# Performance work log

Hardware: AMD Instinct MI355X
Metric: run time of the kernel (lower is better)

The kernel has to match this reference:

```python
import jax, jax.numpy as jnp
import numpy as np

B, T, S, D = 32, 1024, 1024, 512
VOCAB = 1000
INSERT_TOK = jnp.array([1, 2], dtype=jnp.int64)


def setup_inputs() -> dict:
    key = jax.random.key(0)
    k1, k2, k3, k4, k5 = jax.random.split(key, 5)
    input_var = jax.random.randint(k1, (B, T), 0, VOCAB, dtype=jnp.int64)
    output = jax.random.normal(k2, (B, T, D), jnp.float32)
    context = jax.random.normal(k3, (B, S, D), jnp.float32)
    # nn.Linear(2*dim, dim): weight [D, 2D], bias [D]
    W = jax.random.normal(k4, (D, 2 * D), jnp.float32) / np.sqrt(2 * D)
    b = jax.random.normal(k5, (D,), jnp.float32) * 0.01
    return {"input_var": input_var, "output": output, "context": context,
            "di": 0, "W": W, "b": b}


def _hard_align(input_var, src_len):
    """Replicates the python double-loop: sequential 'inserted' counter per batch.
    Returns (j, valid): j[b,i] = column of the 1.0 in attn row i (torch negative
    indices wrapped), valid[b,i] = whether row i gets any 1.0 at all."""
    bsz, tgt_len = input_var.shape
    flags = jnp.isin(input_var, INSERT_TOK)  # [B,T] is token an insert token

    def step(inserted, xi):
        i, flag = xi  # i: scalar position, flag: [B]
        cond = (src_len >= i - inserted)                    # gate, per batch
        ins2 = inserted + jnp.where(cond & flag, 1, 0)      # increment before write
        j = i - ins2 - 1
        j = jnp.where(j < 0, j + src_len, j)                # torch negative-index wrap
        return ins2, (j, cond)

    idxs = jnp.arange(1, tgt_len, dtype=jnp.int32)
    init = jnp.zeros((bsz,), jnp.int32)  # init_inserted()
    _, (j_rows, valid) = jax.lax.scan(step, init, (idxs, flags[:, 1:].T))
    j_rows = j_rows.T      # [B,T-1]
    valid = valid.T        # [B,T-1]
    # row 0: attn[b,0,0] = 1.0 always
    j_full = jnp.concatenate([jnp.zeros((bsz, 1), j_rows.dtype), j_rows], axis=1)
    valid_full = jnp.concatenate([jnp.ones((bsz, 1), bool), valid], axis=1)
    return j_full, valid_full


def reference(input_var, output, context, di, W, b):
    bsz, tgt_len, hid = output.shape
    src_len = context.shape[1]
    j, valid = _hard_align(input_var, src_len)              # [B,T], [B,T]
    vf = valid[:, :, None].astype(output.dtype)
    # hard one-hot attention matrix (as the module materializes it)
    attn = jax.nn.one_hot(j, src_len, dtype=output.dtype) * vf  # [B,T,S]
    # mix = bmm(attn, context) == masked gather of context rows
    mix = jnp.take_along_axis(context, j[:, :, None].astype(jnp.int32), axis=1) * vf
    combined = jnp.concatenate([mix, output], axis=-1)      # [B,T,2D]
    out = jnp.tanh(combined @ W.T + b)                      # [B,T,D]
    return out, attn
```

## Files before the change

### kernel.cpp

```cpp
#include <hip/hip_runtime.h>
#include <hip/hip_bf16.h>

#define B_ 32
#define T_ 1024
#define S_ 1024
#define D_ 512
#define M_ (B_*T_)
#define N_ D_
#define K_ (2*D_)

typedef __attribute__((ext_vector_type(8))) short bf16x8;
typedef __attribute__((ext_vector_type(4))) float f32x4;

__device__ inline unsigned short f2bf(float x) {
    union { float f; unsigned u; } v; v.f = x;
    unsigned r = v.u + 0x7FFFu + ((v.u >> 16) & 1u);
    return (unsigned short)(r >> 16);
}

__device__ inline unsigned cvt2bf(float lo, float hi) {
#if __has_builtin(__builtin_amdgcn_cvt_pk_bf16_f32)
    typedef __attribute__((ext_vector_type(2))) __bf16 bf2;
    union { bf2 v; unsigned u; } r;
    r.v = __builtin_amdgcn_cvt_pk_bf16_f32(lo, hi);
    return r.u;
#else
    return (unsigned)f2bf(lo) | ((unsigned)f2bf(hi) << 16);
#endif
}

__device__ inline float fast_tanh(float x) {
#if __has_builtin(__builtin_amdgcn_exp2f) && __has_builtin(__builtin_amdgcn_rcpf)
    const float e = __builtin_amdgcn_exp2f(x * 2.885390082f);
    const float r = __builtin_amdgcn_rcpf(e + 1.0f);
    return 1.0f - 2.0f * r;
#else
    return tanhf(x);
#endif
}

__global__ void align_kernel(const int* __restrict__ iv, int* __restrict__ jbuf) {
    const int b = blockIdx.x;
    const int lane = threadIdx.x;
    const int* row = iv + b * T_;
    int f[16];
    int local = 0;
    const int t0 = lane * 16;
    #pragma unroll
    for (int q = 0; q < 16; ++q) {
        const int t = t0 + q;
        const int tok = row[t];
        const int fl = (t > 0 && (tok == 1 || tok == 2)) ? 1 : 0;
        f[q] = fl;
        local += fl;
    }
    int incl = local;
    #pragma unroll
    for (int off = 1; off < 64; off <<= 1) {
        const int up = __shfl_up(incl, off, 64);
        if (lane >= off) incl += up;
    }
    int run = incl - local;
    #pragma unroll
    for (int q = 0; q < 16; ++q) {
        const int t = t0 + q;
        run += f[q];
        int j;
        if (t == 0) {
            j = 0;
        } else {
            j = t - run - 1;
            if (j < 0) j += S_;
        }
        jbuf[b * T_ + t] = j;
    }
}

__global__ void pack_w(const float* __restrict__ W, unsigned short* __restrict__ Wbf) {
    const int idx = blockIdx.x * blockDim.x + threadIdx.x;
    const f32x4 a = ((const f32x4*)W)[idx * 2];
    const f32x4 c = ((const f32x4*)W)[idx * 2 + 1];
    union { bf16x8 v; unsigned u[4]; } pk;
    pk.u[0] = cvt2bf(a[0], a[1]); pk.u[1] = cvt2bf(a[2], a[3]);
    pk.u[2] = cvt2bf(c[0], c[1]); pk.u[3] = cvt2bf(c[2], c[3]);
    *(bf16x8*)(Wbf + (size_t)idx * 8) = pk.v;
}

#define BM 128
#define BN 128
#define BK 64
#define NIT (K_ / BK)
#define KMAX (K_ - BK)
#define NGEMM ((M_ / BM) * (N_ / BN))
#define NATTN 512

__global__ __launch_bounds__(256, 2)
void gemm_attn(const unsigned short* __restrict__ Wbf,
               const float* __restrict__ bias,
               float* __restrict__ out,
               float* __restrict__ attn,
               const float* __restrict__ ctx,
               const float* __restrict__ outp,
               const int* __restrict__ jbuf) {
    const int bx = blockIdx.x;
    const int tid = threadIdx.x;

    if (bx < NATTN) {
        const int m0 = bx * 64;
        #pragma unroll 4
        for (int r = 0; r < 64; ++r) {
            const int row = m0 + r;
            const int j = jbuf[row];
            f32x4 v = {0.f, 0.f, 0.f, 0.f};
            if ((j >> 2) == tid) v[j & 3] = 1.0f;
            __builtin_nontemporal_store(v, ((f32x4*)(attn + (size_t)row * S_)) + tid);
        }
        return;
    }

    __shared__ unsigned short As[2][BM * BK];
    __shared__ unsigned short Bs[2][BN * BK];

    const int gbx  = bx - NATTN;
    const int lane = tid & 63;
    const int wave = tid >> 6;
    const int wm = wave >> 1, wn = wave & 1;
    const int l16 = lane & 15, quad = lane >> 4;

    const int bm = gbx & 255;
    const int bn = gbx >> 8;
    const int mBase = bm * BM;
    const int nBase = bn * BN;

    const int kc   = tid & 7;
    const int rsub = tid >> 3;
    const int sw   = kc ^ (rsub & 7);
    const float* actx[4];
    const float* aout[4];
    #pragma unroll
    for (int it = 0; it < 4; ++it) {
        const int r = it * 32 + rsub;
        const int m = mBase + r;
        const int jm = jbuf[m];
        actx[it] = ctx + ((size_t)((m >> 10) * S_ + jm)) * D_ + kc * 8;
        aout[it] = outp + (size_t)m * D_ - D_ + kc * 8;
    }

    f32x4 acc[4][4] = {};
    f32x4 fa0[4][2], fa1[4][2];

#define LOAD_A(FA, KO) do {                                                    \
    const int _koa = (KO);                                                     \
    _Pragma("unroll")                                                          \
    for (int _it = 0; _it < 4; ++_it) {                                        \
        const float* _src = (_koa < D_) ? (actx[_it] + _koa) : (aout[_it] + _koa); \
        FA[_it][0] = ((const f32x4*)_src)[0];                                  \
        FA[_it][1] = ((const f32x4*)_src)[1];                                  \
    }                                                                          \
} while (0)

#define DMA_B(PP, KO) do {                                                     \
    const int _kob = (KO);                                                     \
    _Pragma("unroll")                                                          \
    for (int _it = 0; _it < 4; ++_it) {                                        \
        const int _chunk = _it * 256 + tid;                                    \
        const int _row = _chunk >> 3;                                          \
        const int _kcb = _chunk & 7;                                           \
        const int _gk8 = (_kcb ^ (_row & 7)) * 8;                              \
        const unsigned short* _gB = Wbf + (size_t)(nBase + _row) * K_ + _kob + _gk8; \
        __builtin_amdgcn_global_load_lds(                                      \
            (const __attribute__((address_space(1))) void*)_gB,                \
            (__attribute__((address_space(3))) void*)(&Bs[PP][_chunk * 8]), 16, 0, 0); \
    }                                                                          \
} while (0)

#define STAGE_A(PP, FA) do {                                                   \
    _Pragma("unroll")                                                          \
    for (int _it = 0; _it < 4; ++_it) {                                        \
        union { bf16x8 v; unsigned u[4]; } _pk;                                \
        _pk.u[0] = cvt2bf(FA[_it][0][0], FA[_it][0][1]);                       \
        _pk.u[1] = cvt2bf(FA[_it][0][2], FA[_it][0][3]);                       \
        _pk.u[2] = cvt2bf(FA[_it][1][0], FA[_it][1][1]);                       \
        _pk.u[3] = cvt2bf(FA[_it][1][2], FA[_it][1][3]);                       \
        *(bf16x8*)&As[PP][(_it * 256 + rsub * 8 + sw) * 8] = _pk.v;            \
    }                                                                          \
} while (0)

#define MFMA_PH(PP) do {                                                       \
    _Pragma("unroll")                                                          \
    for (int _ks = 0; _ks < 2; ++_ks) {                                        \
        bf16x8 _af[4], _bfr[4];                                                \
        _Pragma("unroll")                                                      \
        for (int _mt = 0; _mt < 4; ++_mt) {                                    \
            const int _r = wm * 64 + _mt * 16 + l16;                           \
            const int _q = _ks * 4 + quad;                                     \
            _af[_mt] = *(const bf16x8*)&As[PP][(_r * 8 + (_q ^ (_r & 7))) * 8]; \
        }                                                                      \
        _Pragma("unroll")                                                      \
        for (int _nt = 0; _nt < 4; ++_nt) {                                    \
            const int _r = wn * 64 + _nt * 16 + l16;                           \
            const int _q = _ks * 4 + quad;                                     \
            _bfr[_nt] = *(const bf16x8*)&Bs[PP][(_r * 8 + (_q ^ (_r & 7))) * 8]; \
        }                                                                      \
        _Pragma("unroll")                                                      \
        for (int _mt = 0; _mt < 4; ++_mt)                                      \
            _Pragma("unroll")                                                  \
            for (int _nt = 0; _nt < 4; ++_nt)                                  \
                acc[_mt][_nt] = __builtin_amdgcn_mfma_f32_16x16x32_bf16(       \
                    _af[_mt], _bfr[_nt], acc[_mt][_nt], 0, 0, 0);              \
    }                                                                          \
} while (0)

    LOAD_A(fa0, 0);
    DMA_B(0, 0);
    __builtin_amdgcn_sched_barrier(0);
    LOAD_A(fa1, BK);
    __builtin_amdgcn_sched_barrier(0);
    STAGE_A(0, fa0);
    asm volatile("s_waitcnt vmcnt(8) lgkmcnt(0)" ::: "memory");
    __builtin_amdgcn_sched_barrier(0);
    __builtin_amdgcn_s_barrier();

    #pragma unroll 1
    for (int i = 0; i < NIT; i += 2) {
        const int ko = i * BK;
        DMA_B(1, ko + BK);
        __builtin_amdgcn_sched_barrier(0);
        {
            const int _ka = (ko + 2 * BK > KMAX) ? KMAX : ko + 2 * BK;
            LOAD_A(fa0, _ka);
        }
        __builtin_amdgcn_sched_barrier(0);
        STAGE_A(1, fa1);
        MFMA_PH(0);
        asm volatile("s_waitcnt vmcnt(8) lgkmcnt(0)" ::: "memory");
        __builtin_amdgcn_sched_barrier(0);
        __builtin_amdgcn_s_barrier();

        {
            const int _kb = (ko + 2 * BK > KMAX) ? KMAX : ko + 2 * BK;
            DMA_B(0, _kb);
        }
        __builtin_amdgcn_sched_barrier(0);
        {
            const int _kcl = (ko + 3 * BK > KMAX) ? KMAX : ko + 3 * BK;
            LOAD_A(fa1, _kcl);
        }
        __builtin_amdgcn_sched_barrier(0);
        STAGE_A(0, fa0);
        MFMA_PH(1);
        asm volatile("s_waitcnt vmcnt(8) lgkmcnt(0)" ::: "memory");
        __builtin_amdgcn_sched_barrier(0);
        __builtin_amdgcn_s_barrier();
    }

#undef LOAD_A
#undef DMA_B
#undef STAGE_A
#undef MFMA_PH

    #pragma unroll
    for (int nt = 0; nt < 4; ++nt) {
        const int n = nBase + wn * 64 + nt * 16 + l16;
        const float bv = bias[n];
        #pragma unroll
        for (int mt = 0; mt < 4; ++mt) {
            #pragma unroll
            for (int r = 0; r < 4; ++r) {
                const int m = mBase + wm * 64 + mt * 16 + quad * 4 + r;
                const float val = fast_tanh(acc[mt][nt][r] + bv);
                __builtin_nontemporal_store(val, &out[(size_t)m * N_ + n]);
            }
        }
    }
}

extern "C" void kernel_launch(void* const* d_in, const int* in_sizes, int n_in,
                              void* d_out, int out_size, void* d_ws, size_t ws_size,
                              hipStream_t stream) {
    const int*   iv   = (const int*)d_in[0];
    const float* outp = (const float*)d_in[1];
    const float* ctx  = (const float*)d_in[2];
    const float* W    = (const float*)d_in[4];
    const float* bias = (const float*)d_in[5];

    float* out  = (float*)d_out;
    float* attn = out + (size_t)M_ * N_;

    int* jbuf = (int*)d_ws;
    unsigned short* Wbf = (unsigned short*)((char*)d_ws + (size_t)M_ * 4);

    align_kernel<<<B_, 64, 0, stream>>>(iv, jbuf);
    pack_w<<<(N_ * K_ / 8) / 256, 256, 0, stream>>>(W, Wbf);
    gemm_attn<<<NGEMM + NATTN, 256, 0, stream>>>(Wbf, bias, out, attn, ctx, outp, jbuf);
}
```

Baseline: 352.0 us.

## Single-buffer LDS to raise occupancy and fold attn writes into GEMM blocks

Replaces the double-buffered LDS tiles with a single buffer and raises the launch-bounds occupancy target from 2 to 4 blocks per CU. The loop is rescheduled to compute, barrier, then refill, with the register-staged A prefetch still in flight. The separate attention one-hot writer blocks are removed, and each GEMM block now writes 32 attn rows before its epilogue. This trades LDS-level overlap and extra barriers for more resident waves, and it spreads the large attn store stream across GEMM blocks.

```diff
diff --git a/kernel.cpp b/kernel.cpp
--- a/kernel.cpp
+++ b/kernel.cpp
@@ -92,9 +92,8 @@
 #define NIT (K_ / BK)
 #define KMAX (K_ - BK)
 #define NGEMM ((M_ / BM) * (N_ / BN))
-#define NATTN 512
-
-__global__ __launch_bounds__(256, 2)
+
+__global__ __launch_bounds__(256, 4)
 void gemm_attn(const unsigned short* __restrict__ Wbf,
                const float* __restrict__ bias,
                float* __restrict__ out,
@@ -102,26 +101,11 @@
                const float* __restrict__ ctx,
                const float* __restrict__ outp,
                const int* __restrict__ jbuf) {
-    const int bx = blockIdx.x;
+    __shared__ unsigned short As[BM * BK];
+    __shared__ unsigned short Bs[BN * BK];
+
+    const int gbx = blockIdx.x;
     const int tid = threadIdx.x;
-
-    if (bx < NATTN) {
-        const int m0 = bx * 64;
-        #pragma unroll 4
-        for (int r = 0; r < 64; ++r) {
-            const int row = m0 + r;
-            const int j = jbuf[row];
-            f32x4 v = {0.f, 0.f, 0.f, 0.f};
-            if ((j >> 2) == tid) v[j & 3] = 1.0f;
-            __builtin_nontemporal_store(v, ((f32x4*)(attn + (size_t)row * S_)) + tid);
-        }
-        return;
-    }
-
-    __shared__ unsigned short As[2][BM * BK];
-    __shared__ unsigned short Bs[2][BN * BK];
-
-    const int gbx  = bx - NATTN;
     const int lane = tid & 63;
     const int wave = tid >> 6;
     const int wm = wave >> 1, wn = wave & 1;
@@ -159,7 +143,7 @@
     }                                                                          \
 } while (0)
 
-#define DMA_B(PP, KO) do {                                                     \
+#define DMA_B(KO) do {                                                         \
     const int _kob = (KO);                                                     \
     _Pragma("unroll")                                                          \
     for (int _it = 0; _it < 4; ++_it) {                                        \
@@ -170,11 +154,11 @@
         const unsigned short* _gB = Wbf + (size_t)(nBase + _row) * K_ + _kob + _gk8; \
         __builtin_amdgcn_global_load_lds(                                      \
             (const __attribute__((address_space(1))) void*)_gB,                \
-            (__attribute__((address_space(3))) void*)(&Bs[PP][_chunk * 8]), 16, 0, 0); \
-    }                                                                          \
-} while (0)
-
-#define STAGE_A(PP, FA) do {                                                   \
+            (__attribute__((address_space(3))) void*)(&Bs[_chunk * 8]), 16, 0, 0); \
+    }                                                                          \
+} while (0)
+
+#define STAGE_A(FA) do {                                                       \
     _Pragma("unroll")                                                          \
     for (int _it = 0; _it < 4; ++_it) {                                        \
         union { bf16x8 v; unsigned u[4]; } _pk;                                \
@@ -182,11 +166,11 @@
         _pk.u[1] = cvt2bf(FA[_it][0][2], FA[_it][0][3]);                       \
         _pk.u[2] = cvt2bf(FA[_it][1][0], FA[_it][1][1]);                       \
         _pk.u[3] = cvt2bf(FA[_it][1][2], FA[_it][1][3]);                       \
-        *(bf16x8*)&As[PP][(_it * 256 + rsub * 8 + sw) * 8] = _pk.v;            \
-    }                                                                          \
-} while (0)
-
-#define MFMA_PH(PP) do {                                                       \
+        *(bf16x8*)&As[(_it * 256 + rsub * 8 + sw) * 8] = _pk.v;                \
+    }                                                                          \
+} while (0)
+
+#define MFMA_PH() do {                                                         \
     _Pragma("unroll")                                                          \
     for (int _ks = 0; _ks < 2; ++_ks) {                                        \
         bf16x8 _af[4], _bfr[4];                                                \
@@ -194,13 +178,13 @@
         for (int _mt = 0; _mt < 4; ++_mt) {                                    \
             const int _r = wm * 64 + _mt * 16 + l16;                           \
             const int _q = _ks * 4 + quad;                                     \
-            _af[_mt] = *(const bf16x8*)&As[PP][(_r * 8 + (_q ^ (_r & 7))) * 8]; \
+            _af[_mt] = *(const bf16x8*)&As[(_r * 8 + (_q ^ (_r & 7))) * 8];    \
         }                                                                      \
         _Pragma("unroll")                                                      \
         for (int _nt = 0; _nt < 4; ++_nt) {                                    \
             const int _r = wn * 64 + _nt * 16 + l16;                           \
             const int _q = _ks * 4 + quad;                                     \
-            _bfr[_nt] = *(const bf16x8*)&Bs[PP][(_r * 8 + (_q ^ (_r & 7))) * 8]; \
+            _bfr[_nt] = *(const bf16x8*)&Bs[(_r * 8 + (_q ^ (_r & 7))) * 8];   \
         }                                                                      \
         _Pragma("unroll")                                                      \
         for (int _mt = 0; _mt < 4; ++_mt)                                      \
@@ -212,11 +196,11 @@
 } while (0)
 
     LOAD_A(fa0, 0);
-    DMA_B(0, 0);
+    DMA_B(0);
     __builtin_amdgcn_sched_barrier(0);
     LOAD_A(fa1, BK);
     __builtin_amdgcn_sched_barrier(0);
-    STAGE_A(0, fa0);
+    STAGE_A(fa0);
     asm volatile("s_waitcnt vmcnt(8) lgkmcnt(0)" ::: "memory");
     __builtin_amdgcn_sched_barrier(0);
     __builtin_amdgcn_s_barrier();
@@ -224,40 +208,59 @@
     #pragma unroll 1
     for (int i = 0; i < NIT; i += 2) {
         const int ko = i * BK;
-        DMA_B(1, ko + BK);
+        MFMA_PH();
+        __builtin_amdgcn_s_barrier();
+        DMA_B(ko + BK);
         __builtin_amdgcn_sched_barrier(0);
         {
             const int _ka = (ko + 2 * BK > KMAX) ? KMAX : ko + 2 * BK;
             LOAD_A(fa0, _ka);
         }
         __builtin_amdgcn_sched_barrier(0);
-        STAGE_A(1, fa1);
-        MFMA_PH(0);
+        STAGE_A(fa1);
         asm volatile("s_waitcnt vmcnt(8) lgkmcnt(0)" ::: "memory");
         __builtin_amdgcn_sched_barrier(0);
         __builtin_amdgcn_s_barrier();
 
-        {
-            const int _kb = (ko + 2 * BK > KMAX) ? KMAX : ko + 2 * BK;
-            DMA_B(0, _kb);
-        }
-        __builtin_amdgcn_sched_barrier(0);
-        {
-            const int _kcl = (ko + 3 * BK > KMAX) ? KMAX : ko + 3 * BK;
-            LOAD_A(fa1, _kcl);
-        }
-        __builtin_amdgcn_sched_barrier(0);
-        STAGE_A(0, fa0);
-        MFMA_PH(1);
-        asm volatile("s_waitcnt vmcnt(8) lgkmcnt(0)" ::: "memory");
-        __builtin_amdgcn_sched_barrier(0);
-        __builtin_amdgcn_s_barrier();
+        MFMA_PH();
+        if (i != NIT - 2) {
+            __builtin_amdgcn_s_barrier();
+            DMA_B(ko + 2 * BK);
+            __builtin_amdgcn_sched_barrier(0);
+            LOAD_A(fa1, ko + 3 * BK);
+            __builtin_amdgcn_sched_barrier(0);
+            STAGE_A(fa0);
+            asm volatile("s_waitcnt vmcnt(8) lgkmcnt(0)" ::: "memory");
+            __builtin_amdgcn_sched_barrier(0);
+            __builtin_amdgcn_s_barrier();
+        }
     }
 
 #undef LOAD_A
 #undef DMA_B
 #undef STAGE_A
 #undef MFMA_PH
+
+    {
+        const int arow = gbx * 32 + (tid >> 3);
+        const int jv = jbuf[arow];
+        const int c4 = jv >> 2;
+        const bool hit = ((c4 & 7) == (tid & 7));
+        const int starget = c4 >> 3;
+        const int elem = jv & 3;
+        f32x4* abase = (f32x4*)(attn + (size_t)arow * S_);
+        #pragma unroll
+        for (int s = 0; s < 32; ++s) {
+            f32x4 v = {0.f, 0.f, 0.f, 0.f};
+            if (hit && s == starget) {
+                v[0] = (elem == 0) ? 1.f : 0.f;
+                v[1] = (elem == 1) ? 1.f : 0.f;
+                v[2] = (elem == 2) ? 1.f : 0.f;
+                v[3] = (elem == 3) ? 1.f : 0.f;
+            }
+            __builtin_nontemporal_store(v, abase + s * 8 + (tid & 7));
+        }
+    }
 
     #pragma unroll
     for (int nt = 0; nt < 4; ++nt) {
@@ -292,5 +295,5 @@
 
     align_kernel<<<B_, 64, 0, stream>>>(iv, jbuf);
     pack_w<<<(N_ * K_ / 8) / 256, 256, 0, stream>>>(W, Wbf);
-    gemm_attn<<<NGEMM + NATTN, 256, 0, stream>>>(Wbf, bias, out, attn, ctx, outp, jbuf);
-}
+    gemm_attn<<<NGEMM, 256, 0, stream>>>(Wbf, bias, out, attn, ctx, outp, jbuf);
+}
```

Result: slower. 422.0 us (+19.9%).

## Enlarge GEMM tiles to 256x256, fold attn one-hot writes into epilogue, XCD-aware block mapping

Applied to the files above, without the earlier changes.

Doubles the GEMM tile to 256x256 with 512 threads (8 waves, each computing 64x128), which halves how often A and B are reloaded across blocks. The separate attention-writing blocks are removed; each GEMM block now writes its share of the one-hot attn rows just before its output epilogue. Block indices are remapped so consecutive blocks spread across the 8 XCDs. The cost is heavier register pressure (the accumulator doubles) and much more LDS, which may lower occupancy, and there are only 256 blocks in total.

```diff
diff --git a/kernel.cpp b/kernel.cpp
--- a/kernel.cpp
+++ b/kernel.cpp
@@ -86,15 +86,14 @@
     *(bf16x8*)(Wbf + (size_t)idx * 8) = pk.v;
 }
 
-#define BM 128
-#define BN 128
+#define BM 256
+#define BN 256
 #define BK 64
 #define NIT (K_ / BK)
 #define KMAX (K_ - BK)
 #define NGEMM ((M_ / BM) * (N_ / BN))
-#define NATTN 512
-
-__global__ __launch_bounds__(256, 2)
+
+__global__ __launch_bounds__(512, 2)
 void gemm_attn(const unsigned short* __restrict__ Wbf,
                const float* __restrict__ bias,
                float* __restrict__ out,
@@ -105,48 +104,37 @@
     const int bx = blockIdx.x;
     const int tid = threadIdx.x;
 
-    if (bx < NATTN) {
-        const int m0 = bx * 64;
-        #pragma unroll 4
-        for (int r = 0; r < 64; ++r) {
-            const int row = m0 + r;
-            const int j = jbuf[row];
-            f32x4 v = {0.f, 0.f, 0.f, 0.f};
-            if ((j >> 2) == tid) v[j & 3] = 1.0f;
-            __builtin_nontemporal_store(v, ((f32x4*)(attn + (size_t)row * S_)) + tid);
-        }
-        return;
-    }
-
     __shared__ unsigned short As[2][BM * BK];
     __shared__ unsigned short Bs[2][BN * BK];
 
-    const int gbx  = bx - NATTN;
     const int lane = tid & 63;
     const int wave = tid >> 6;
     const int wm = wave >> 1, wn = wave & 1;
     const int l16 = lane & 15, quad = lane >> 4;
 
-    const int bm = gbx & 255;
-    const int bn = gbx >> 8;
+    const int xcd = bx & 7;
+    const int bn  = (bx >> 3) & 1;
+    const int bm  = ((bx >> 4) << 3) | xcd;
     const int mBase = bm * BM;
     const int nBase = bn * BN;
 
-    const int kc   = tid & 7;
+    const int g    = tid & 7;
     const int rsub = tid >> 3;
-    const int sw   = kc ^ (rsub & 7);
+    const int sw   = g ^ (rsub & 7);
     const float* actx[4];
     const float* aout[4];
+    const unsigned short* bSrc[4];
     #pragma unroll
     for (int it = 0; it < 4; ++it) {
-        const int r = it * 32 + rsub;
+        const int r = it * 64 + rsub;
         const int m = mBase + r;
         const int jm = jbuf[m];
-        actx[it] = ctx + ((size_t)((m >> 10) * S_ + jm)) * D_ + kc * 8;
-        aout[it] = outp + (size_t)m * D_ - D_ + kc * 8;
-    }
-
-    f32x4 acc[4][4] = {};
+        actx[it] = ctx + ((size_t)((m >> 10) * S_ + jm)) * D_ + g * 8;
+        aout[it] = outp + (size_t)m * D_ - D_ + g * 8;
+        bSrc[it] = Wbf + (size_t)(nBase + r) * K_ + sw * 8;
+    }
+
+    f32x4 acc[4][8] = {};
     f32x4 fa0[4][2], fa1[4][2];
 
 #define LOAD_A(FA, KO) do {                                                    \
@@ -159,22 +147,18 @@
     }                                                                          \
 } while (0)
 
-#define DMA_B(PP, KO) do {                                                     \
+#define DMA_B(P, KO) do {                                                      \
     const int _kob = (KO);                                                     \
     _Pragma("unroll")                                                          \
     for (int _it = 0; _it < 4; ++_it) {                                        \
-        const int _chunk = _it * 256 + tid;                                    \
-        const int _row = _chunk >> 3;                                          \
-        const int _kcb = _chunk & 7;                                           \
-        const int _gk8 = (_kcb ^ (_row & 7)) * 8;                              \
-        const unsigned short* _gB = Wbf + (size_t)(nBase + _row) * K_ + _kob + _gk8; \
         __builtin_amdgcn_global_load_lds(                                      \
-            (const __attribute__((address_space(1))) void*)_gB,                \
-            (__attribute__((address_space(3))) void*)(&Bs[PP][_chunk * 8]), 16, 0, 0); \
-    }                                                                          \
-} while (0)
-
-#define STAGE_A(PP, FA) do {                                                   \
+            (const __attribute__((address_space(1))) void*)(bSrc[_it] + _kob), \
+            (__attribute__((address_space(3))) void*)(&Bs[P][(_it * 512 + tid) * 8]), \
+            16, 0, 0);                                                         \
+    }                                                                          \
+} while (0)
+
+#define STAGE_A(P, FA) do {                                                    \
     _Pragma("unroll")                                                          \
     for (int _it = 0; _it < 4; ++_it) {                                        \
         union { bf16x8 v; unsigned u[4]; } _pk;                                \
@@ -182,30 +166,29 @@
         _pk.u[1] = cvt2bf(FA[_it][0][2], FA[_it][0][3]);                       \
         _pk.u[2] = cvt2bf(FA[_it][1][0], FA[_it][1][1]);                       \
         _pk.u[3] = cvt2bf(FA[_it][1][2], FA[_it][1][3]);                       \
-        *(bf16x8*)&As[PP][(_it * 256 + rsub * 8 + sw) * 8] = _pk.v;            \
-    }                                                                          \
-} while (0)
-
-#define MFMA_PH(PP) do {                                                       \
+        *(bf16x8*)&As[P][(_it * 512 + rsub * 8 + sw) * 8] = _pk.v;             \
+    }                                                                          \
+} while (0)
+
+#define MFMA_PH(P) do {                                                        \
     _Pragma("unroll")                                                          \
     for (int _ks = 0; _ks < 2; ++_ks) {                                        \
-        bf16x8 _af[4], _bfr[4];                                                \
+        bf16x8 _af[4], _bfr[8];                                                \
+        const int _q = _ks * 4 + quad;                                         \
         _Pragma("unroll")                                                      \
         for (int _mt = 0; _mt < 4; ++_mt) {                                    \
             const int _r = wm * 64 + _mt * 16 + l16;                           \
-            const int _q = _ks * 4 + quad;                                     \
-            _af[_mt] = *(const bf16x8*)&As[PP][(_r * 8 + (_q ^ (_r & 7))) * 8]; \
+            _af[_mt] = *(const bf16x8*)&As[P][(_r * 8 + (_q ^ (_r & 7))) * 8]; \
         }                                                                      \
         _Pragma("unroll")                                                      \
-        for (int _nt = 0; _nt < 4; ++_nt) {                                    \
-            const int _r = wn * 64 + _nt * 16 + l16;                           \
-            const int _q = _ks * 4 + quad;                                     \
-            _bfr[_nt] = *(const bf16x8*)&Bs[PP][(_r * 8 + (_q ^ (_r & 7))) * 8]; \
+        for (int _nt = 0; _nt < 8; ++_nt) {                                    \
+            const int _rb = wn * 128 + _nt * 16 + l16;                         \
+            _bfr[_nt] = *(const bf16x8*)&Bs[P][(_rb * 8 + (_q ^ (_rb & 7))) * 8]; \
         }                                                                      \
         _Pragma("unroll")                                                      \
         for (int _mt = 0; _mt < 4; ++_mt)                                      \
             _Pragma("unroll")                                                  \
-            for (int _nt = 0; _nt < 4; ++_nt)                                  \
+            for (int _nt = 0; _nt < 8; ++_nt)                                  \
                 acc[_mt][_nt] = __builtin_amdgcn_mfma_f32_16x16x32_bf16(       \
                     _af[_mt], _bfr[_nt], acc[_mt][_nt], 0, 0, 0);              \
     }                                                                          \
@@ -220,38 +203,35 @@
     asm volatile("s_waitcnt vmcnt(8) lgkmcnt(0)" ::: "memory");
     __builtin_amdgcn_sched_barrier(0);
     __builtin_amdgcn_s_barrier();
+    __builtin_amdgcn_sched_barrier(0);
 
     #pragma unroll 1
     for (int i = 0; i < NIT; i += 2) {
         const int ko = i * BK;
+        const int k2 = (ko + 2 * BK > KMAX) ? KMAX : ko + 2 * BK;
+        const int k3 = (ko + 3 * BK > KMAX) ? KMAX : ko + 3 * BK;
+
         DMA_B(1, ko + BK);
         __builtin_amdgcn_sched_barrier(0);
-        {
-            const int _ka = (ko + 2 * BK > KMAX) ? KMAX : ko + 2 * BK;
-            LOAD_A(fa0, _ka);
-        }
+        LOAD_A(fa0, k2);
         __builtin_amdgcn_sched_barrier(0);
         STAGE_A(1, fa1);
         MFMA_PH(0);
         asm volatile("s_waitcnt vmcnt(8) lgkmcnt(0)" ::: "memory");
         __builtin_amdgcn_sched_barrier(0);
         __builtin_amdgcn_s_barrier();
-
-        {
-            const int _kb = (ko + 2 * BK > KMAX) ? KMAX : ko + 2 * BK;
-            DMA_B(0, _kb);
-        }
-        __builtin_amdgcn_sched_barrier(0);
-        {
-            const int _kcl = (ko + 3 * BK > KMAX) ? KMAX : ko + 3 * BK;
-            LOAD_A(fa1, _kcl);
-        }
+        __builtin_amdgcn_sched_barrier(0);
+
+        DMA_B(0, k2);
+        __builtin_amdgcn_sched_barrier(0);
+        LOAD_A(fa1, k3);
         __builtin_amdgcn_sched_barrier(0);
         STAGE_A(0, fa0);
         MFMA_PH(1);
         asm volatile("s_waitcnt vmcnt(8) lgkmcnt(0)" ::: "memory");
         __builtin_amdgcn_sched_barrier(0);
         __builtin_amdgcn_s_barrier();
+        __builtin_amdgcn_sched_barrier(0);
     }
 
 #undef LOAD_A
@@ -259,9 +239,23 @@
 #undef STAGE_A
 #undef MFMA_PH
 
-    #pragma unroll
-    for (int nt = 0; nt < 4; ++nt) {
-        const int n = nBase + wn * 64 + nt * 16 + l16;
+    {
+        const int aBase = mBase + bn * 128;
+        const int col  = tid & 255;
+        const int half = tid >> 8;
+        #pragma unroll 4
+        for (int r = 0; r < 64; ++r) {
+            const int row = aBase + r * 2 + half;
+            const int j = jbuf[row];
+            f32x4 v = {0.f, 0.f, 0.f, 0.f};
+            if ((j >> 2) == col) v[j & 3] = 1.0f;
+            __builtin_nontemporal_store(v, ((f32x4*)(attn + (size_t)row * S_)) + col);
+        }
+    }
+
+    #pragma unroll
+    for (int nt = 0; nt < 8; ++nt) {
+        const int n = nBase + wn * 128 + nt * 16 + l16;
         const float bv = bias[n];
         #pragma unroll
         for (int mt = 0; mt < 4; ++mt) {
@@ -292,5 +286,5 @@
 
     align_kernel<<<B_, 64, 0, stream>>>(iv, jbuf);
     pack_w<<<(N_ * K_ / 8) / 256, 256, 0, stream>>>(W, Wbf);
-    gemm_attn<<<NGEMM + NATTN, 256, 0, stream>>>(Wbf, bias, out, attn, ctx, outp, jbuf);
-}
+    gemm_attn<<<NGEMM, 512, 0, stream>>>(Wbf, bias, out, attn, ctx, outp, jbuf);
+}
```

Result: slower. 370.8 us (+5.3%).
